# Kernel optimization log

Measured on AMD Instinct MI355X. Metric: run time of the kernel, lower is better.

The kernel has to match this reference:

```python
import jax, jax.numpy as jnp
import numpy as np

B, CIN, H, W = 16, 1024, 32, 32
WIDTH = 256          # bottleneck width = planes * base_width/64 * cardinality
OUT = 1024           # planes * expansion
HEADS = WIDTH // 8   # 32
KS = 3               # kernel_size of SelfAttLayer


def unfold3x3(x):
    # x: (B, C, H, W) -> (B, C, 9, H, W), torch.nn.Unfold(3, padding=1) ordering (row-major kernel)
    xp = jnp.pad(x, ((0, 0), (0, 0), (1, 1), (1, 1)))
    h, w = x.shape[2], x.shape[3]
    patches = [xp[:, :, i:i + h, j:j + w] for i in range(KS) for j in range(KS)]
    return jnp.stack(patches, axis=2)


def bn(x, s, b):
    # inference-mode BatchNorm2d with running stats folded into per-channel scale/bias
    return x * s[None, :, None, None] + b[None, :, None, None]


def conv1x1(x, w):
    # w: (Cout, Cin)
    return jnp.einsum('bchw,oc->bohw', x, w)


def setup_inputs() -> dict:
    key = jax.random.key(0)
    ks = jax.random.split(key, 16)
    f = lambda k, shp, scale: (jax.random.normal(k, shp, dtype=jnp.float32) * scale)
    inp = {
        'x': f(ks[0], (B, CIN, H, W), 1.0),
        'w_conv1': f(ks[1], (WIDTH, CIN), 1.0 / np.sqrt(CIN)),
        'bn1_s': jnp.ones((WIDTH,), jnp.float32), 'bn1_b': jnp.zeros((WIDTH,), jnp.float32),
        'wq': f(ks[2], (WIDTH, WIDTH), 1.0 / np.sqrt(WIDTH)),
        'bnq_s': jnp.ones((WIDTH,), jnp.float32), 'bnq_b': jnp.zeros((WIDTH,), jnp.float32),
        'wk': f(ks[3], (WIDTH, WIDTH), 1.0 / np.sqrt(WIDTH)),
        'bnk_s': jnp.ones((WIDTH,), jnp.float32), 'bnk_b': jnp.zeros((WIDTH,), jnp.float32),
        'wv': f(ks[4], (WIDTH, WIDTH), 1.0 / np.sqrt(WIDTH)),
        'bnv_s': jnp.ones((WIDTH,), jnp.float32), 'bnv_b': jnp.zeros((WIDTH,), jnp.float32),
        'pos_h': f(ks[5], (WIDTH, KS, 1), 1.0),
        'pos_w': f(ks[6], (WIDTH, 1, KS), 1.0),
        'bnatt_s': jnp.ones((WIDTH,), jnp.float32), 'bnatt_b': jnp.zeros((WIDTH,), jnp.float32),
        'w_conv3': f(ks[7], (OUT, WIDTH), 1.0 / np.sqrt(WIDTH)),
        'bn3_s': jnp.ones((OUT,), jnp.float32), 'bn3_b': jnp.zeros((OUT,), jnp.float32),
    }
    return inp


def self_att(x, wq, bnq_s, bnq_b, wk, bnk_s, bnk_b, wv, bnv_s, bnv_b,
             pos_h, pos_w, bnatt_s, bnatt_b):
    b, c, h, w = x.shape
    d = c // HEADS
    q = jax.nn.relu(bn(conv1x1(x, wq), bnq_s, bnq_b))          # (B,C,H,W)
    k = jax.nn.relu(bn(conv1x1(x, wk), bnk_s, bnk_b))          # key_ks=1 -> 1x1 conv
    v = bn(conv1x1(x, wv), bnv_s, bnv_b)
    unfold_k = unfold3x3(k)                                     # (B,C,9,H,W)
    pos = (pos_h + pos_w).reshape(1, c, KS * KS, 1, 1)          # (1,C,9,1,1)
    kp = (unfold_k + pos).reshape(b, HEADS, d, KS * KS, h, w)
    qh = q.reshape(b, HEADS, d, h, w)
    attn = jnp.einsum('bgdhw,bgdkhw->bgkhw', qh, kp)            # (B,heads,9,H,W)
    attn = jax.nn.softmax(attn, axis=2)
    # local conv: each channel-group of size d shares its head's attention weights
    v_unf = unfold3x3(v).reshape(b, HEADS, d, KS * KS, h, w)
    out = jnp.einsum('bgdkhw,bgkhw->bgdhw', v_unf, attn).reshape(b, c, h, w)
    return jax.nn.relu(bn(out, bnatt_s, bnatt_b))


def reference(x, w_conv1, bn1_s, bn1_b, wq, bnq_s, bnq_b, wk, bnk_s, bnk_b,
              wv, bnv_s, bnv_b, pos_h, pos_w, bnatt_s, bnatt_b,
              w_conv3, bn3_s, bn3_b):
    residual = x
    h = jax.nn.relu(bn(conv1x1(x, w_conv1), bn1_s, bn1_b))
    h = self_att(h, wq, bnq_s, bnq_b, wk, bnk_s, bnk_b, wv, bnv_s, bnv_b,
                 pos_h, pos_w, bnatt_s, bnatt_b)
    h = bn(conv1x1(h, w_conv3), bn3_s, bn3_b)
    return jax.nn.relu(h + residual)
```

## Files before the change

### kernel.cpp

```cpp
#include <hip/hip_runtime.h>
#include <stdint.h>


typedef __attribute__((ext_vector_type(4))) float f32x4;
typedef __attribute__((ext_vector_type(8))) __bf16 bf16x8;
typedef __attribute__((ext_vector_type(4))) unsigned short u16x4;
typedef __attribute__((ext_vector_type(8))) unsigned short u16x8;

__device__ __forceinline__ float bf2f(unsigned short u) {
  union { unsigned int i; float f; } c; c.i = ((unsigned int)u) << 16; return c.f;
}
__device__ __forceinline__ unsigned short f2bf(float f) {
  union { float f; unsigned int i; } c; c.f = f;
  unsigned int x = c.i;
  return (unsigned short)((x + 0x7FFFu + ((x >> 16) & 1u)) >> 16);
}
__device__ __forceinline__ void gload_lds16(const unsigned short* g, unsigned short* l) {
  __builtin_amdgcn_global_load_lds(
      (const __attribute__((address_space(1))) unsigned int*)(const void*)g,
      (__attribute__((address_space(3))) unsigned int*)(void*)l, 16, 0, 0);
}

__global__ void k_convert(const float* __restrict__ w1, const float* __restrict__ wq,
                          const float* __restrict__ wk, const float* __restrict__ wv,
                          const float* __restrict__ w3,
                          const float* __restrict__ sq, const float* __restrict__ sk,
                          const float* __restrict__ sv, const float* __restrict__ bq,
                          const float* __restrict__ bk, const float* __restrict__ bv,
                          unsigned short* __restrict__ w1b, unsigned short* __restrict__ wqkvb,
                          unsigned short* __restrict__ w3b, float* __restrict__ sqkv,
                          float* __restrict__ bqkv) {
  const int idx = blockIdx.x * 256 + threadIdx.x;
  if (idx < 262144) { w1b[idx] = f2bf(w1[idx]); return; }
  if (idx < 327680) { wqkvb[idx - 262144] = f2bf(wq[idx - 262144]); return; }
  if (idx < 393216) { wqkvb[idx - 262144] = f2bf(wk[idx - 327680]); return; }
  if (idx < 458752) { wqkvb[idx - 262144] = f2bf(wv[idx - 393216]); return; }
  if (idx < 720896) { w3b[idx - 458752] = f2bf(w3[idx - 458752]); return; }
  if (idx < 721664) {
    const int i = idx - 720896;
    sqkv[i] = i < 256 ? sq[i] : (i < 512 ? sk[i - 256] : sv[i - 512]);
    return;
  }
  if (idx < 722432) {
    const int i = idx - 721664;
    bqkv[i] = i < 256 ? bq[i] : (i < 512 ? bk[i - 256] : bv[i - 512]);
  }
}

__global__ __launch_bounds__(256) void k_transpose_x(const float* __restrict__ x,
                                                     unsigned short* __restrict__ xt) {
  __shared__ float tile[32][33];
  const int b  = blockIdx.z;
  const int c0 = blockIdx.y * 32;
  const int p0 = blockIdx.x * 32;
  const int tx = threadIdx.x & 31;
  const int ty = threadIdx.x >> 5;
  const float* xb = x + (size_t)b * 1048576;
  unsigned short* xtb = xt + (size_t)b * 1048576;
#pragma unroll
  for (int i = 0; i < 4; ++i)
    tile[ty + i * 8][tx] = xb[(size_t)(c0 + ty + i * 8) * 1024 + p0 + tx];
  __syncthreads();
#pragma unroll
  for (int i = 0; i < 4; ++i)
    xtb[(size_t)(p0 + ty + i * 8) * 1024 + c0 + tx] = f2bf(tile[tx][ty + i * 8]);
}

template <int MODE>
__global__ __launch_bounds__(256, 4) void k_gemm64(
    const unsigned short* __restrict__ A, const unsigned short* __restrict__ B,
    void* __restrict__ CoutV, const float* __restrict__ scale,
    const float* __restrict__ bias, const float* __restrict__ resid,
    int K, int relu_mask) {
  __shared__ unsigned short lA[64 * 32];
  __shared__ unsigned short lB[64 * 32];
  const int m0 = blockIdx.y * 64;
  const int n0 = blockIdx.x * 64;
  const int tid = threadIdx.x;
  const int lane = tid & 63, wid = tid >> 6;
  const int wm = (wid >> 1) * 32, wn = (wid & 1) * 32;
  const int fr = lane & 15, fq = lane >> 4;

  f32x4 acc[2][2] = {};

  const unsigned short* Asrc = A + (size_t)(m0 + wid * 16 + (lane >> 2)) * K + (lane & 3) * 8;
  const unsigned short* Bsrc = B + (size_t)(n0 + wid * 16 + (lane >> 2)) * K + (lane & 3) * 8;
  unsigned short* lAw = &lA[wid * 512];
  unsigned short* lBw = &lB[wid * 512];

  float rres[2][2][4];
  if (MODE == 1) {
#pragma unroll
    for (int i = 0; i < 2; ++i) {
      const int og = m0 + wm + i * 16 + fq * 4;
#pragma unroll
      for (int j = 0; j < 2; ++j) {
        const int P = n0 + wn + j * 16 + fr;
        const size_t base = (size_t)(P >> 10) * 1048576 + (size_t)(P & 1023);
#pragma unroll
        for (int rr = 0; rr < 4; ++rr)
          rres[i][j][rr] = resid[base + (size_t)(og + rr) * 1024];
      }
    }
  }

  for (int k0 = 0; k0 < K; k0 += 32) {
    gload_lds16(Asrc + k0, lAw);
    gload_lds16(Bsrc + k0, lBw);
    __syncthreads();

    bf16x8 af[2], bb[2];
#pragma unroll
    for (int i = 0; i < 2; ++i)
      af[i] = *(const bf16x8*)&lA[(wm + i * 16 + fr) * 32 + fq * 8];
#pragma unroll
    for (int j = 0; j < 2; ++j)
      bb[j] = *(const bf16x8*)&lB[(wn + j * 16 + fr) * 32 + fq * 8];
#pragma unroll
    for (int i = 0; i < 2; ++i)
#pragma unroll
      for (int j = 0; j < 2; ++j)
        acc[i][j] = __builtin_amdgcn_mfma_f32_16x16x32_bf16(af[i], bb[j], acc[i][j], 0, 0, 0);
    __syncthreads();
  }

#pragma unroll
  for (int i = 0; i < 2; ++i) {
    const int og = m0 + wm + i * 16 + fq * 4;
    const f32x4 s4 = *(const f32x4*)&scale[og];
    const f32x4 b4 = *(const f32x4*)&bias[og];
#pragma unroll
    for (int j = 0; j < 2; ++j) {
      const int P = n0 + wn + j * 16 + fr;
      if (MODE == 0) {
        unsigned short* Cout = (unsigned short*)CoutV;
        const int do_relu = (relu_mask >> (og >> 8)) & 1;
        const size_t obase = (size_t)(og >> 8) * 4194304 + (size_t)P * 256 + (og & 255);
        u16x4 pk;
#pragma unroll
        for (int rr = 0; rr < 4; ++rr) {
          float v = acc[i][j][rr] * s4[rr] + b4[rr];
          if (do_relu) v = fmaxf(v, 0.0f);
          pk[rr] = f2bf(v);
        }
        *(u16x4*)&Cout[obase] = pk;
      } else {
        float* Cout = (float*)CoutV;
        const size_t base = (size_t)(P >> 10) * 1048576 + (size_t)(P & 1023);
#pragma unroll
        for (int rr = 0; rr < 4; ++rr) {
          float v = acc[i][j][rr] * s4[rr] + b4[rr] + rres[i][j][rr];
          Cout[base + (size_t)(og + rr) * 1024] = fmaxf(v, 0.0f);
        }
      }
    }
  }
}

__global__ __launch_bounds__(256, 4) void k_attn(
    const unsigned short* __restrict__ Q, const unsigned short* __restrict__ Kb,
    const unsigned short* __restrict__ Vb, unsigned short* __restrict__ O,
    const float* __restrict__ pos_h, const float* __restrict__ pos_w,
    const float* __restrict__ bs, const float* __restrict__ bb) {
  __shared__ float ph_l[3][256];
  __shared__ float pw_l[3][256];
  {
    const int c = threadIdx.x;
#pragma unroll
    for (int i = 0; i < 3; ++i) {
      ph_l[i][c] = pos_h[c * 3 + i];
      pw_l[i][c] = pos_w[c * 3 + i];
    }
  }
  __syncthreads();
  const int tid = threadIdx.x;
  const int g = tid & 31, s = tid >> 5;
  const int P = blockIdx.x * 8 + s;
  const int b = P >> 10, pix = P & 1023;
  const int hh = pix >> 5, ww = pix & 31;
  const int c0 = g * 8;

  float qf[8];
  {
    u16x8 qv = *(const u16x8*)&Q[(size_t)P * 256 + c0];
#pragma unroll
    for (int d = 0; d < 8; ++d) qf[d] = bf2f(qv[d]);
  }
  float Ai[3], Bj[3];
#pragma unroll
  for (int i = 0; i < 3; ++i) {
    float a = 0.f, w = 0.f;
#pragma unroll
    for (int d = 0; d < 8; ++d) {
      a += qf[d] * ph_l[i][c0 + d];
      w += qf[d] * pw_l[i][c0 + d];
    }
    Ai[i] = a; Bj[i] = w;
  }

  float S[9];
  int nPs[9];
#pragma unroll
  for (int t = 0; t < 9; ++t) {
    const int di = t / 3, dj = t % 3;
    const int nh = hh + di - 1, nw = ww + dj - 1;
    float sum = Ai[di] + Bj[dj];
    int nP = -1;
    if ((unsigned)nh < 32u && (unsigned)nw < 32u) {
      nP = (b << 10) + (nh << 5) + nw;
      u16x8 kv = *(const u16x8*)&Kb[(size_t)nP * 256 + c0];
#pragma unroll
      for (int d = 0; d < 8; ++d) sum += qf[d] * bf2f(kv[d]);
    }
    nPs[t] = nP;
    S[t] = sum;
  }

  float mx = S[0];
#pragma unroll
  for (int t = 1; t < 9; ++t) mx = fmaxf(mx, S[t]);
  float e[9], tot = 0.f;
#pragma unroll
  for (int t = 0; t < 9; ++t) { e[t] = __expf(S[t] - mx); tot += e[t]; }
  const float inv = 1.0f / tot;

  float of[8] = {0.f, 0.f, 0.f, 0.f, 0.f, 0.f, 0.f, 0.f};
#pragma unroll
  for (int t = 0; t < 9; ++t) {
    if (nPs[t] >= 0) {
      u16x8 vv = *(const u16x8*)&Vb[(size_t)nPs[t] * 256 + c0];
      const float w = e[t] * inv;
#pragma unroll
      for (int d = 0; d < 8; ++d) of[d] += w * bf2f(vv[d]);
    }
  }

  u16x8 res;
#pragma unroll
  for (int d = 0; d < 8; ++d) {
    float v = of[d] * bs[c0 + d] + bb[c0 + d];
    v = fmaxf(v, 0.0f);
    res[d] = f2bf(v);
  }
  *(u16x8*)&O[(size_t)P * 256 + c0] = res;
}

extern "C" void kernel_launch(void* const* d_in, const int* in_sizes, int n_in,
                              void* d_out, int out_size, void* d_ws, size_t ws_size,
                              hipStream_t stream) {
  (void)in_sizes; (void)n_in; (void)out_size; (void)ws_size;
  const float* x       = (const float*)d_in[0];
  const float* w1      = (const float*)d_in[1];
  const float* bn1_s   = (const float*)d_in[2];
  const float* bn1_b   = (const float*)d_in[3];
  const float* wq      = (const float*)d_in[4];
  const float* bnq_s   = (const float*)d_in[5];
  const float* bnq_b   = (const float*)d_in[6];
  const float* wk      = (const float*)d_in[7];
  const float* bnk_s   = (const float*)d_in[8];
  const float* bnk_b   = (const float*)d_in[9];
  const float* wv      = (const float*)d_in[10];
  const float* bnv_s   = (const float*)d_in[11];
  const float* bnv_b   = (const float*)d_in[12];
  const float* pos_h   = (const float*)d_in[13];
  const float* pos_w   = (const float*)d_in[14];
  const float* bnatt_s = (const float*)d_in[15];
  const float* bnatt_b = (const float*)d_in[16];
  const float* w3      = (const float*)d_in[17];
  const float* bn3_s   = (const float*)d_in[18];
  const float* bn3_b   = (const float*)d_in[19];

  char* ws = (char*)d_ws;
  unsigned short* h1t   = (unsigned short*)(ws);
  unsigned short* qkvt  = (unsigned short*)(ws + 8388608);
  unsigned short* att   = (unsigned short*)(ws + 33554432);
  unsigned short* xt    = (unsigned short*)(ws + 41943040);
  unsigned short* w1b   = (unsigned short*)(ws + 75497472);
  unsigned short* wqkvb = (unsigned short*)(ws + 76021760);
  unsigned short* w3b   = (unsigned short*)(ws + 76414976);
  float*          sqkv  = (float*)(ws + 76939264);
  float*          bqkv  = (float*)(ws + 76942336);

  k_convert<<<dim3(2822), dim3(256), 0, stream>>>(
      w1, wq, wk, wv, w3, bnq_s, bnk_s, bnv_s, bnq_b, bnk_b, bnv_b,
      w1b, wqkvb, w3b, sqkv, bqkv);

  k_transpose_x<<<dim3(32, 32, 16), dim3(256), 0, stream>>>(x, xt);

  k_gemm64<0><<<dim3(256, 4), dim3(256), 0, stream>>>(
      w1b, xt, h1t, bn1_s, bn1_b, nullptr, 1024, 1);

  k_gemm64<0><<<dim3(256, 12), dim3(256), 0, stream>>>(
      wqkvb, h1t, qkvt, sqkv, bqkv, nullptr, 256, 3);

  k_attn<<<dim3(2048), dim3(256), 0, stream>>>(
      qkvt, qkvt + 4194304, qkvt + 8388608, att, pos_h, pos_w, bnatt_s, bnatt_b);

  k_gemm64<1><<<dim3(256, 16), dim3(256), 0, stream>>>(
      w3b, att, d_out, bn3_s, bn3_b, x, 256, 0);
}
```

Baseline: 112.4 us.

## Template GEMM tile sizes per layer and XOR-swizzle LDS layout

Generalizes the 64x64 GEMM into a templated kernel with configurable per-warp MFMA fragment counts, giving larger block tiles (64x128, 128x128, 128x64) for the three 1x1 convolutions. The larger tiles raise data reuse and cut global-to-LDS traffic per FLOP. An XOR swizzle of the 8-element column group is applied to both the global->LDS write and the fragment read to reduce LDS bank conflicts. The trade-offs are fewer blocks per GEMM, a lower launch-bounds occupancy hint (3 instead of 4), and more accumulator registers.

```diff
diff --git a/kernel.cpp b/kernel.cpp
--- a/kernel.cpp
+++ b/kernel.cpp
@@ -66,35 +66,41 @@
     xtb[(size_t)(p0 + ty + i * 8) * 1024 + c0 + tx] = f2bf(tile[tx][ty + i * 8]);
 }
 
-template <int MODE>
-__global__ __launch_bounds__(256, 4) void k_gemm64(
+template <int MF, int NF, int MODE>
+__global__ __launch_bounds__(256, 3) void k_gemm_bt(
     const unsigned short* __restrict__ A, const unsigned short* __restrict__ B,
     void* __restrict__ CoutV, const float* __restrict__ scale,
     const float* __restrict__ bias, const float* __restrict__ resid,
     int K, int relu_mask) {
-  __shared__ unsigned short lA[64 * 32];
-  __shared__ unsigned short lB[64 * 32];
-  const int m0 = blockIdx.y * 64;
-  const int n0 = blockIdx.x * 64;
+  constexpr int BM = MF * 32, BN = NF * 32;
+  __shared__ unsigned short lA[BM * 32];
+  __shared__ unsigned short lB[BN * 32];
+  const int m0 = blockIdx.y * BM;
+  const int n0 = blockIdx.x * BN;
   const int tid = threadIdx.x;
   const int lane = tid & 63, wid = tid >> 6;
-  const int wm = (wid >> 1) * 32, wn = (wid & 1) * 32;
+  const int wm = (wid >> 1) * (MF * 16), wn = (wid & 1) * (NF * 16);
   const int fr = lane & 15, fq = lane >> 4;
-
-  f32x4 acc[2][2] = {};
-
-  const unsigned short* Asrc = A + (size_t)(m0 + wid * 16 + (lane >> 2)) * K + (lane & 3) * 8;
-  const unsigned short* Bsrc = B + (size_t)(n0 + wid * 16 + (lane >> 2)) * K + (lane & 3) * 8;
-  unsigned short* lAw = &lA[wid * 512];
-  unsigned short* lBw = &lB[wid * 512];
-
-  float rres[2][2][4];
+  const int cgr = (fq ^ (fr & 3)) * 8;
+
+  f32x4 acc[MF][NF] = {};
+
+  const int sr  = lane >> 2;
+  const int scg = ((lane & 3) ^ (sr & 3)) * 8;
+  const int warA = wid * (MF * 8);
+  const int warB = wid * (NF * 8);
+  const unsigned short* Asrc = A + (size_t)(m0 + warA + sr) * K + scg;
+  const unsigned short* Bsrc = B + (size_t)(n0 + warB + sr) * K + scg;
+  unsigned short* lAw = &lA[warA * 32];
+  unsigned short* lBw = &lB[warB * 32];
+
+  float rres[MF][NF][4];
   if (MODE == 1) {
 #pragma unroll
-    for (int i = 0; i < 2; ++i) {
+    for (int i = 0; i < MF; ++i) {
       const int og = m0 + wm + i * 16 + fq * 4;
 #pragma unroll
-      for (int j = 0; j < 2; ++j) {
+      for (int j = 0; j < NF; ++j) {
         const int P = n0 + wn + j * 16 + fr;
         const size_t base = (size_t)(P >> 10) * 1048576 + (size_t)(P & 1023);
 #pragma unroll
@@ -105,32 +111,36 @@
   }
 
   for (int k0 = 0; k0 < K; k0 += 32) {
-    gload_lds16(Asrc + k0, lAw);
-    gload_lds16(Bsrc + k0, lBw);
+#pragma unroll
+    for (int u = 0; u < MF / 2; ++u)
+      gload_lds16(Asrc + (size_t)u * 16 * K + k0, lAw + u * 512);
+#pragma unroll
+    for (int u = 0; u < NF / 2; ++u)
+      gload_lds16(Bsrc + (size_t)u * 16 * K + k0, lBw + u * 512);
     __syncthreads();
 
-    bf16x8 af[2], bb[2];
-#pragma unroll
-    for (int i = 0; i < 2; ++i)
-      af[i] = *(const bf16x8*)&lA[(wm + i * 16 + fr) * 32 + fq * 8];
-#pragma unroll
-    for (int j = 0; j < 2; ++j)
-      bb[j] = *(const bf16x8*)&lB[(wn + j * 16 + fr) * 32 + fq * 8];
-#pragma unroll
-    for (int i = 0; i < 2; ++i)
-#pragma unroll
-      for (int j = 0; j < 2; ++j)
+    bf16x8 af[MF], bb[NF];
+#pragma unroll
+    for (int i = 0; i < MF; ++i)
+      af[i] = *(const bf16x8*)&lA[(wm + i * 16 + fr) * 32 + cgr];
+#pragma unroll
+    for (int j = 0; j < NF; ++j)
+      bb[j] = *(const bf16x8*)&lB[(wn + j * 16 + fr) * 32 + cgr];
+#pragma unroll
+    for (int i = 0; i < MF; ++i)
+#pragma unroll
+      for (int j = 0; j < NF; ++j)
         acc[i][j] = __builtin_amdgcn_mfma_f32_16x16x32_bf16(af[i], bb[j], acc[i][j], 0, 0, 0);
     __syncthreads();
   }
 
 #pragma unroll
-  for (int i = 0; i < 2; ++i) {
+  for (int i = 0; i < MF; ++i) {
     const int og = m0 + wm + i * 16 + fq * 4;
     const f32x4 s4 = *(const f32x4*)&scale[og];
     const f32x4 b4 = *(const f32x4*)&bias[og];
 #pragma unroll
-    for (int j = 0; j < 2; ++j) {
+    for (int j = 0; j < NF; ++j) {
       const int P = n0 + wn + j * 16 + fr;
       if (MODE == 0) {
         unsigned short* Cout = (unsigned short*)CoutV;
@@ -287,15 +297,15 @@
 
   k_transpose_x<<<dim3(32, 32, 16), dim3(256), 0, stream>>>(x, xt);
 
-  k_gemm64<0><<<dim3(256, 4), dim3(256), 0, stream>>>(
+  k_gemm_bt<2, 4, 0><<<dim3(128, 4), dim3(256), 0, stream>>>(
       w1b, xt, h1t, bn1_s, bn1_b, nullptr, 1024, 1);
 
-  k_gemm64<0><<<dim3(256, 12), dim3(256), 0, stream>>>(
+  k_gemm_bt<4, 4, 0><<<dim3(128, 6), dim3(256), 0, stream>>>(
       wqkvb, h1t, qkvt, sqkv, bqkv, nullptr, 256, 3);
 
   k_attn<<<dim3(2048), dim3(256), 0, stream>>>(
       qkvt, qkvt + 4194304, qkvt + 8388608, att, pos_h, pos_w, bnatt_s, bnatt_b);
 
-  k_gemm64<1><<<dim3(256, 16), dim3(256), 0, stream>>>(
+  k_gemm_bt<4, 2, 1><<<dim3(256, 8), dim3(256), 0, stream>>>(
       w3b, att, d_out, bn3_s, bn3_b, x, 256, 0);
 }
```

Result: faster. 109.6 us (-2.5%).
